# Kernel optimization log

Measured on AMD Instinct MI355X. Metric: run time of the kernel, lower is better.

## Reference

```python
import jax, jax.numpy as jnp
import numpy as np

B, S, D, H = 4, 2048, 1024, 16
DK = D // H
DFF = 4 * D
EPS = 1e-6


def setup_inputs() -> dict:
    key = jax.random.key(0)
    ks = jax.random.split(key, 16)
    s = 0.02
    return {
        "x": jax.random.normal(ks[0], (B, S, D), jnp.float32),
        "mask": jax.random.randint(ks[1], (B, 1, 1, S), 0, 2, jnp.int32),
        "wq": jax.random.normal(ks[2], (D, D), jnp.float32) * s,
        "bq": jnp.zeros((D,), jnp.float32),
        "wk": jax.random.normal(ks[3], (D, D), jnp.float32) * s,
        "bk": jnp.zeros((D,), jnp.float32),
        "wv": jax.random.normal(ks[4], (D, D), jnp.float32) * s,
        "bv": jnp.zeros((D,), jnp.float32),
        "wo": jax.random.normal(ks[5], (D, D), jnp.float32) * s,
        "bo": jnp.zeros((D,), jnp.float32),
        "w1": jax.random.normal(ks[6], (DFF, D), jnp.float32) * s,
        "b1": jnp.zeros((DFF,), jnp.float32),
        "w2": jax.random.normal(ks[7], (D, DFF), jnp.float32) * s,
        "b2": jnp.zeros((D,), jnp.float32),
        "a1": jnp.ones((1,), jnp.float32),
        "c1": jnp.zeros((1,), jnp.float32),
        "a2": jnp.ones((1,), jnp.float32),
        "c2": jnp.zeros((1,), jnp.float32),
    }


def _layernorm(x, alpha, bias):
    # source: alpha * (x - mean) / (std + eps) + bias, torch std is unbiased
    mean = jnp.mean(x, axis=-1, keepdims=True)
    std = jnp.std(x, axis=-1, keepdims=True, ddof=1)
    return alpha * (x - mean) / (std + EPS) + bias


def _mha(x, mask, wq, bq, wk, bk, wv, bv, wo, bo):
    q = (x @ wq.T + bq).reshape(B, S, H, DK).transpose(0, 2, 1, 3)  # [B,H,S,DK]
    k = (x @ wk.T + bk).reshape(B, S, H, DK).transpose(0, 2, 1, 3)
    v = (x @ wv.T + bv).reshape(B, S, H, DK).transpose(0, 2, 1, 3)
    scores = jnp.einsum("bhqd,bhkd->bhqk", q, k) / jnp.sqrt(jnp.float32(DK))
    scores = jnp.where(mask == 0, jnp.float32(-1e9), scores)
    attn = jax.nn.softmax(scores, axis=-1)
    out = jnp.einsum("bhqk,bhkd->bhqd", attn, v)  # [B,H,S,DK]
    out = out.transpose(0, 2, 1, 3).reshape(B, S, D)
    return out @ wo.T + bo


def reference(x, mask, wq, bq, wk, bk, wv, bv, wo, bo, w1, b1, w2, b2, a1, c1, a2, c2):
    # residual 1: x + MHA(LN(x))  (dropout = identity in eval)
    h = x + _mha(_layernorm(x, a1, c1), mask, wq, bq, wk, bk, wv, bv, wo, bo)
    # residual 2: h + FFN(LN(h))
    hn = _layernorm(h, a2, c2)
    ffn = jax.nn.relu(hn @ w1.T + b1) @ w2.T + b2
    return h + ffn
```

## Files before the change

### kernel.cpp

```cpp
#include <hip/hip_runtime.h>
#include <math.h>

static constexpr int B  = 4;
static constexpr int S  = 2048;
static constexpr int D  = 1024;
static constexpr int H  = 16;
static constexpr int DFF = 4096;

typedef __attribute__((ext_vector_type(8))) short short8;
typedef __attribute__((ext_vector_type(8))) unsigned short ushort8;
typedef __attribute__((ext_vector_type(4))) unsigned short ushort4v;
typedef __attribute__((ext_vector_type(4))) float f32x4;

__device__ __forceinline__ float b2f(unsigned short u) {
  unsigned int x = ((unsigned int)u) << 16;
  float f;
  __builtin_memcpy(&f, &x, 4);
  return f;
}
__device__ __forceinline__ unsigned short f2b(float f) {
  unsigned int x;
  __builtin_memcpy(&x, &f, 4);
  x += 0x7fffu + ((x >> 16) & 1u);
  return (unsigned short)(x >> 16);
}

__device__ __forceinline__ f32x4 mfma16(short8 a, short8 b, f32x4 c) {
  return __builtin_amdgcn_mfma_f32_16x16x32_bf16(a, b, c, 0, 0, 0);
}

__device__ __forceinline__ void gload_lds16(const void* gsrc, void* ldst) {
  __builtin_amdgcn_global_load_lds(
      (__attribute__((address_space(1))) void*)(uintptr_t)gsrc,
      (__attribute__((address_space(3))) void*)ldst, 16, 0, 0);
}

struct CvtArgs {
  const float* s[6];
  unsigned short* d[6];
  int n[6];
};
__global__ __launch_bounds__(256) void convert6(CvtArgs a) {
  const int seg = blockIdx.y;
  const int i = (blockIdx.x * 256 + threadIdx.x) * 4;
  if (i < a.n[seg]) {
    f32x4 v = *(const f32x4*)(a.s[seg] + i);
    ushort4v o;
#pragma unroll
    for (int j = 0; j < 4; j++) o[j] = f2b(v[j]);
    *(ushort4v*)(a.d[seg] + i) = o;
  }
}

__global__ __launch_bounds__(256) void ln_fused(const float* __restrict__ x,
                                                const float* __restrict__ ap,
                                                const float* __restrict__ cp,
                                                unsigned short* __restrict__ out) {
  const int row = blockIdx.x, tid = threadIdx.x;
  const size_t base = (size_t)row * D;
  float v[4];
  float s = 0.f, sq = 0.f;
#pragma unroll
  for (int i = 0; i < 4; i++) {
    v[i] = x[base + tid + i * 256];
    s += v[i];
    sq += v[i] * v[i];
  }
#pragma unroll
  for (int o = 32; o > 0; o >>= 1) {
    s += __shfl_xor(s, o);
    sq += __shfl_xor(sq, o);
  }
  __shared__ __align__(16) float rs[4], rq[4];
  const int wave = tid >> 6, lane = tid & 63;
  if (lane == 0) {
    rs[wave] = s;
    rq[wave] = sq;
  }
  __syncthreads();
  const float S1 = rs[0] + rs[1] + rs[2] + rs[3];
  const float S2 = rq[0] + rq[1] + rq[2] + rq[3];
  const float mean = S1 * (1.f / 1024.f);
  const float var = fmaxf(0.f, (S2 - 1024.f * mean * mean) * (1.f / 1023.f));
  const float rstd = 1.f / (sqrtf(var) + 1e-6f);
  const float alpha = ap[0], beta = cp[0];
#pragma unroll
  for (int i = 0; i < 4; i++)
    out[base + tid + i * 256] = f2b(alpha * (v[i] - mean) * rstd + beta);
}

template <int EPI>
__global__ __launch_bounds__(256) void gemm_bb(
    const unsigned short* __restrict__ A, const unsigned short* __restrict__ W,
    const float* __restrict__ bias0, const float* __restrict__ bias1,
    const float* __restrict__ bias2, const float* __restrict__ resid,
    void* __restrict__ out, unsigned short* __restrict__ outK,
    unsigned short* __restrict__ outV, int M, int N, int K, int ldw) {
  __shared__ __align__(16) unsigned short As[128 * 32];
  __shared__ __align__(16) unsigned short Bs[128 * 32];
  const int tid = threadIdx.x;
  const int lane = tid & 63, wave = tid >> 6;
  const int quad = lane >> 4, l16 = lane & 15;
  const int m0 = blockIdx.y * 128, n0 = blockIdx.x * 128;
  const int wm = (wave >> 1) * 64, wn = (wave & 1) * 64;

  f32x4 acc[4][4];
#pragma unroll
  for (int i = 0; i < 4; i++)
#pragma unroll
    for (int j = 0; j < 4; j++) acc[i][j] = {0.f, 0.f, 0.f, 0.f};

  const int rA = tid >> 2;
  const int kc = (tid & 3) * 8;

  for (int k0 = 0; k0 < K; k0 += 32) {
    __syncthreads();
#pragma unroll
    for (int i = 0; i < 2; i++) {
      const int row = i * 64 + rA;
      gload_lds16(&A[(size_t)(m0 + row) * K + k0 + kc], &As[(i * 256 + wave * 64) * 8]);
      gload_lds16(&W[(size_t)(n0 + row) * ldw + k0 + kc], &Bs[(i * 256 + wave * 64) * 8]);
    }
    __syncthreads();
    short8 af[4], bf[4];
#pragma unroll
    for (int t = 0; t < 4; t++) {
      af[t] = *(const short8*)&As[(wm + t * 16 + l16) * 32 + quad * 8];
      bf[t] = *(const short8*)&Bs[(wn + t * 16 + l16) * 32 + quad * 8];
    }
#pragma unroll
    for (int mt = 0; mt < 4; mt++)
#pragma unroll
      for (int nt = 0; nt < 4; nt++) acc[mt][nt] = mfma16(af[mt], bf[nt], acc[mt][nt]);
  }

  if (EPI == 4) {
    const int band = (n0 + wn) >> 10;
    const float* bp = band == 0 ? bias0 : (band == 1 ? bias1 : bias2);
#pragma unroll
    for (int nt = 0; nt < 4; nt++) {
      const int col = n0 + wn + nt * 16 + l16;
      const int cl = col & 1023;
      const float bv = bp[cl];
#pragma unroll
      for (int mt = 0; mt < 4; mt++) {
#pragma unroll
        for (int r = 0; r < 4; r++) {
          const int row = m0 + wm + mt * 16 + quad * 4 + r;
          const float v = acc[mt][nt][r] + bv;
          if (band == 0)
            ((unsigned short*)out)[(size_t)row * 1024 + cl] = f2b(v);
          else if (band == 1)
            outK[(size_t)row * 1024 + cl] = f2b(v);
          else
            outV[((size_t)((row >> 11) * 1024 + cl)) * 2048 + (row & 2047)] = f2b(v);
        }
      }
    }
  } else {
#pragma unroll
    for (int nt = 0; nt < 4; nt++) {
      const int col = n0 + wn + nt * 16 + l16;
      const float bv = (EPI == 3) ? 0.f : bias0[col];
#pragma unroll
      for (int mt = 0; mt < 4; mt++) {
#pragma unroll
        for (int r = 0; r < 4; r++) {
          const int row = m0 + wm + mt * 16 + quad * 4 + r;
          const size_t idx = (size_t)row * N + col;
          float v = acc[mt][nt][r] + bv;
          if (EPI == 2) {
            v = fmaxf(v, 0.f);
            ((unsigned short*)out)[idx] = f2b(v);
          } else {
            v += resid[idx];
            ((float*)out)[idx] = v;
          }
        }
      }
    }
  }
}

__global__ __launch_bounds__(256) void attn_kernel(unsigned short* __restrict__ Q,
                                                   const unsigned short* __restrict__ Kb,
                                                   const unsigned short* __restrict__ VT,
                                                   const int* __restrict__ mask) {
  constexpr int PAD = 72;
  __shared__ __align__(16) unsigned short Ks[64 * PAD];
  __shared__ __align__(16) unsigned short VTs[64 * PAD];
  __shared__ __align__(16) unsigned short Pb[4][16 * PAD];

  const int tid = threadIdx.x, lane = tid & 63, wave = tid >> 6;
  const int quad = lane >> 4, l16 = lane & 15;
  const int q0 = blockIdx.x * 64;
  const int b = blockIdx.y >> 4, h = blockIdx.y & 15;

  short8 qf0, qf1;
  {
    const int qr = q0 + wave * 16 + l16;
    const unsigned short* qp = &Q[((size_t)(b * S) + qr) * D + h * 64 + quad * 8];
    qf0 = *(const short8*)qp;
    qf1 = *(const short8*)(qp + 32);
  }

  float l_acc = 0.f;
  f32x4 o_acc[4];
#pragma unroll
  for (int t = 0; t < 4; t++) o_acc[t] = {0.f, 0.f, 0.f, 0.f};

  const int rT = tid >> 3;
  const int cT = (tid & 7) * 8;

  for (int kt = 0; kt < S / 64; kt++) {
    const int k0 = kt * 64;
    ushort8 kv[2], vv[2];
#pragma unroll
    for (int i = 0; i < 2; i++) {
      const int r = i * 32 + rT;
      kv[i] = *(const ushort8*)&Kb[((size_t)(b * S) + k0 + r) * D + h * 64 + cT];
      vv[i] = *(const ushort8*)&VT[((size_t)(blockIdx.y * 64 + r)) * S + k0 + cT];
    }
    __syncthreads();
#pragma unroll
    for (int i = 0; i < 2; i++) {
      const int r = i * 32 + rT;
      *(ushort8*)&Ks[r * PAD + cT] = kv[i];
      *(ushort8*)&VTs[r * PAD + cT] = vv[i];
    }
    __syncthreads();

    f32x4 sc[4];
#pragma unroll
    for (int nt = 0; nt < 4; nt++) sc[nt] = {0.f, 0.f, 0.f, 0.f};
#pragma unroll
    for (int nt = 0; nt < 4; nt++) {
      short8 kf0 = *(const short8*)&Ks[(nt * 16 + l16) * PAD + quad * 8];
      short8 kf1 = *(const short8*)&Ks[(nt * 16 + l16) * PAD + 32 + quad * 8];
      sc[nt] = mfma16(kf0, qf0, sc[nt]);
      sc[nt] = mfma16(kf1, qf1, sc[nt]);
    }

#pragma unroll
    for (int nt = 0; nt < 4; nt++) {
      const int4 mv = *(const int4*)&mask[b * S + k0 + nt * 16 + quad * 4];
      ushort4v pk;
      {
        const float p0 = __expf(fmaf(sc[nt][0], 0.125f, mv.x ? -12.f : -42.f));
        const float p1 = __expf(fmaf(sc[nt][1], 0.125f, mv.y ? -12.f : -42.f));
        const float p2 = __expf(fmaf(sc[nt][2], 0.125f, mv.z ? -12.f : -42.f));
        const float p3 = __expf(fmaf(sc[nt][3], 0.125f, mv.w ? -12.f : -42.f));
        l_acc += p0 + p1 + p2 + p3;
        pk[0] = f2b(p0);
        pk[1] = f2b(p1);
        pk[2] = f2b(p2);
        pk[3] = f2b(p3);
      }
      *(ushort4v*)&Pb[wave][l16 * PAD + nt * 16 + quad * 4] = pk;
    }

    short8 pf0 = *(const short8*)&Pb[wave][l16 * PAD + quad * 8];
    short8 pf1 = *(const short8*)&Pb[wave][l16 * PAD + 32 + quad * 8];
#pragma unroll
    for (int nt = 0; nt < 4; nt++) {
      short8 vf0 = *(const short8*)&VTs[(nt * 16 + l16) * PAD + quad * 8];
      short8 vf1 = *(const short8*)&VTs[(nt * 16 + l16) * PAD + 32 + quad * 8];
      o_acc[nt] = mfma16(pf0, vf0, o_acc[nt]);
      o_acc[nt] = mfma16(pf1, vf1, o_acc[nt]);
    }
  }

  l_acc += __shfl_xor(l_acc, 16);
  l_acc += __shfl_xor(l_acc, 32);

#pragma unroll
  for (int r = 0; r < 4; r++) {
    const float lr = __shfl(l_acc, quad * 4 + r);
    const float inv = 1.f / lr;
    const int q = q0 + wave * 16 + quad * 4 + r;
#pragma unroll
    for (int nt = 0; nt < 4; nt++) {
      const int dk = nt * 16 + l16;
      Q[((size_t)(b * S) + q) * D + h * 64 + dk] = f2b(o_acc[nt][r] * inv);
    }
  }
}

__global__ __launch_bounds__(256) void stats_kernel(const float* __restrict__ x,
                                                    float2* __restrict__ st) {
  const int row = blockIdx.x, tid = threadIdx.x;
  const size_t base = (size_t)row * D;
  float s = 0.f, sq = 0.f;
#pragma unroll
  for (int i = 0; i < 4; i++) {
    const float v = x[base + tid + i * 256];
    s += v;
    sq += v * v;
  }
#pragma unroll
  for (int o = 32; o > 0; o >>= 1) {
    s += __shfl_xor(s, o);
    sq += __shfl_xor(sq, o);
  }
  __shared__ __align__(16) float rs[4], rq[4];
  const int wave = tid >> 6, lane = tid & 63;
  if (lane == 0) {
    rs[wave] = s;
    rq[wave] = sq;
  }
  __syncthreads();
  if (tid == 0) {
    const float S1 = rs[0] + rs[1] + rs[2] + rs[3];
    const float S2 = rq[0] + rq[1] + rq[2] + rq[3];
    const float mean = S1 * (1.f / 1024.f);
    const float var = fmaxf(0.f, (S2 - 1024.f * mean * mean) * (1.f / 1023.f));
    const float rstd = 1.f / (sqrtf(var) + 1e-6f);
    st[row] = make_float2(mean, rstd);
  }
}

template <int EPI, int NORM, int AF32, int OUTF32>
__global__ __launch_bounds__(256) void gemm_bt(
    const void* __restrict__ Ap, const float* __restrict__ W,
    const float* __restrict__ bias, const float* __restrict__ resid,
    void* __restrict__ outp, const float2* __restrict__ stats,
    const float* __restrict__ alpha_p, const float* __restrict__ beta_p,
    int M, int N, int K, int ldw) {
  __shared__ __align__(16) unsigned short As[128 * 32];
  __shared__ __align__(16) unsigned short Bs[128 * 32];
  const int tid = threadIdx.x;
  const int lane = tid & 63, wave = tid >> 6;
  const int quad = lane >> 4, l16 = lane & 15;
  const int m0 = blockIdx.y * 128, n0 = blockIdx.x * 128;
  const int wm = (wave >> 1) * 64, wn = (wave & 1) * 64;

  float alpha = 0.f, beta = 0.f;
  if (NORM) {
    alpha = alpha_p[0];
    beta = beta_p[0];
  }

  f32x4 acc[4][4];
#pragma unroll
  for (int i = 0; i < 4; i++)
#pragma unroll
    for (int j = 0; j < 4; j++) acc[i][j] = {0.f, 0.f, 0.f, 0.f};

  const int rA = tid >> 2;
  const int kc = (tid & 3) * 8;

  for (int k0 = 0; k0 < K; k0 += 32) {
    ushort8 av[2], bv8[2];
#pragma unroll
    for (int i = 0; i < 2; i++) {
      const int row = i * 64 + rA;
      if (AF32) {
        const float* ap = (const float*)Ap + (size_t)(m0 + row) * K + k0 + kc;
        f32x4 a0 = *(const f32x4*)ap;
        f32x4 a1 = *(const f32x4*)(ap + 4);
        if (NORM) {
          const float2 st = stats[m0 + row];
#pragma unroll
          for (int j = 0; j < 4; j++) {
            a0[j] = alpha * (a0[j] - st.x) * st.y + beta;
            a1[j] = alpha * (a1[j] - st.x) * st.y + beta;
          }
        }
#pragma unroll
        for (int j = 0; j < 4; j++) {
          av[i][j] = f2b(a0[j]);
          av[i][j + 4] = f2b(a1[j]);
        }
      } else {
        av[i] = *(const ushort8*)((const unsigned short*)Ap +
                                  (size_t)(m0 + row) * K + k0 + kc);
      }
      const float* wp = W + (size_t)(n0 + row) * ldw + k0 + kc;
      f32x4 w0 = *(const f32x4*)wp;
      f32x4 w1 = *(const f32x4*)(wp + 4);
#pragma unroll
      for (int j = 0; j < 4; j++) {
        bv8[i][j] = f2b(w0[j]);
        bv8[i][j + 4] = f2b(w1[j]);
      }
    }
    __syncthreads();
#pragma unroll
    for (int i = 0; i < 2; i++) {
      const int row = i * 64 + rA;
      *(ushort8*)&As[row * 32 + kc] = av[i];
      *(ushort8*)&Bs[row * 32 + kc] = bv8[i];
    }
    __syncthreads();
    short8 af[4], bf[4];
#pragma unroll
    for (int t = 0; t < 4; t++) {
      af[t] = *(const short8*)&As[(wm + t * 16 + l16) * 32 + quad * 8];
      bf[t] = *(const short8*)&Bs[(wn + t * 16 + l16) * 32 + quad * 8];
    }
#pragma unroll
    for (int mt = 0; mt < 4; mt++)
#pragma unroll
      for (int nt = 0; nt < 4; nt++) acc[mt][nt] = mfma16(af[mt], bf[nt], acc[mt][nt]);
  }

#pragma unroll
  for (int nt = 0; nt < 4; nt++) {
    const int col = n0 + wn + nt * 16 + l16;
    const float bv = (EPI == 3) ? 0.f : bias[col];
#pragma unroll
    for (int mt = 0; mt < 4; mt++) {
#pragma unroll
      for (int r = 0; r < 4; r++) {
        const int row = m0 + wm + mt * 16 + quad * 4 + r;
        float v = acc[mt][nt][r] + bv;
        if (EPI == 2) v = fmaxf(v, 0.f);
        if (EPI == 4) {
          const size_t vtidx =
              ((size_t)((row >> 11) * 1024 + col)) * 2048 + (row & 2047);
          ((unsigned short*)outp)[vtidx] = f2b(v);
        } else {
          const size_t idx = (size_t)row * N + col;
          if (EPI == 1 || EPI == 3) v += resid[idx];
          if (OUTF32)
            ((float*)outp)[idx] = v;
          else
            ((unsigned short*)outp)[idx] = f2b(v);
        }
      }
    }
  }
}

extern "C" void kernel_launch(void* const* d_in, const int* in_sizes, int n_in,
                              void* d_out, int out_size, void* d_ws, size_t ws_size,
                              hipStream_t stream) {
  (void)in_sizes; (void)n_in; (void)out_size;
  const float* x  = (const float*)d_in[0];
  const int* mask = (const int*)d_in[1];
  const float* wq = (const float*)d_in[2];
  const float* bq = (const float*)d_in[3];
  const float* wk = (const float*)d_in[4];
  const float* bk = (const float*)d_in[5];
  const float* wv = (const float*)d_in[6];
  const float* bv = (const float*)d_in[7];
  const float* wo = (const float*)d_in[8];
  const float* bo = (const float*)d_in[9];
  const float* w1 = (const float*)d_in[10];
  const float* b1 = (const float*)d_in[11];
  const float* w2 = (const float*)d_in[12];
  const float* b2 = (const float*)d_in[13];
  const float* a1 = (const float*)d_in[14];
  const float* c1 = (const float*)d_in[15];
  const float* a2 = (const float*)d_in[16];
  const float* c2 = (const float*)d_in[17];

  char* ws = (char*)d_ws;
  const size_t MB = 1 << 20;
  const int M = B * S;
  dim3 blk(256);
  dim3 gAttn(S / 64, B * H);

  if (ws_size >= 89 * MB) {
    const int tier3 = (ws_size >= 152 * MB);
    const int tier2 = (ws_size >= 121 * MB);
    unsigned short* wqkv_b = (unsigned short*)(ws + 0);
    unsigned short* wo_b   = (unsigned short*)(ws + 6 * MB);
    unsigned short* w1_b   = (unsigned short*)(ws + 8 * MB);
    unsigned short* w2_b   = (unsigned short*)(ws + 16 * MB);
    unsigned short* ln1x   = (unsigned short*)(ws + 25 * MB);
    unsigned short* q      = (unsigned short*)(ws + 41 * MB);
    unsigned short* kk     = (unsigned short*)(ws + 57 * MB);
    unsigned short* vt     = (unsigned short*)(ws + 73 * MB);
    float*          hbuf   = (float*)(ws + 57 * MB);
    unsigned short* ln2x   = (unsigned short*)(ws + 25 * MB);
    unsigned short* ffn1q  = (unsigned short*)(ws + 41 * MB);
    unsigned short* ffn1h  = (unsigned short*)(ws + 89 * MB);
    unsigned short* ffn1f  = (unsigned short*)(ws + 89 * MB);
    float* outb = (float*)d_out;

    CvtArgs ca;
    ca.s[0] = wq; ca.d[0] = wqkv_b;            ca.n[0] = 1048576;
    ca.s[1] = wk; ca.d[1] = wqkv_b + 1048576;  ca.n[1] = 1048576;
    ca.s[2] = wv; ca.d[2] = wqkv_b + 2097152;  ca.n[2] = 1048576;
    ca.s[3] = wo; ca.d[3] = wo_b;              ca.n[3] = 1048576;
    ca.s[4] = w1; ca.d[4] = w1_b;              ca.n[4] = 4194304;
    ca.s[5] = w2; ca.d[5] = w2_b;              ca.n[5] = 4194304;
    convert6<<<dim3(4096, 6), blk, 0, stream>>>(ca);

    ln_fused<<<M, blk, 0, stream>>>(x, a1, c1, ln1x);
    gemm_bb<4><<<dim3(24, 64), blk, 0, stream>>>(ln1x, wqkv_b, bq, bk, bv, nullptr,
                                                 q, kk, vt, M, 3072, D, D);
    attn_kernel<<<gAttn, blk, 0, stream>>>(q, kk, vt, mask);
    gemm_bb<1><<<dim3(8, 64), blk, 0, stream>>>(q, wo_b, bo, nullptr, nullptr, x,
                                                hbuf, nullptr, nullptr, M, D, D, D);
    ln_fused<<<M, blk, 0, stream>>>(hbuf, a2, c2, ln2x);

    if (tier3) {
      gemm_bb<2><<<dim3(32, 64), blk, 0, stream>>>(ln2x, w1_b, b1, nullptr, nullptr,
                                                   nullptr, ffn1f, nullptr, nullptr,
                                                   M, DFF, D, D);
      gemm_bb<1><<<dim3(8, 64), blk, 0, stream>>>(ffn1f, w2_b, b2, nullptr, nullptr,
                                                  hbuf, outb, nullptr, nullptr,
                                                  M, D, DFF, DFF);
    } else if (tier2) {
      gemm_bb<2><<<dim3(16, 64), blk, 0, stream>>>(ln2x, w1_b, b1, nullptr, nullptr,
                                                   nullptr, ffn1h, nullptr, nullptr,
                                                   M, 2048, D, D);
      gemm_bb<1><<<dim3(8, 64), blk, 0, stream>>>(ffn1h, w2_b, b2, nullptr, nullptr,
                                                  hbuf, outb, nullptr, nullptr,
                                                  M, D, 2048, DFF);
      gemm_bb<2><<<dim3(16, 64), blk, 0, stream>>>(ln2x, w1_b + (size_t)2048 * D,
                                                   b1 + 2048, nullptr, nullptr, nullptr,
                                                   ffn1h, nullptr, nullptr, M, 2048, D, D);
      gemm_bb<3><<<dim3(8, 64), blk, 0, stream>>>(ffn1h, w2_b + 2048, nullptr, nullptr,
                                                  nullptr, outb, outb, nullptr, nullptr,
                                                  M, D, 2048, DFF);
    } else {
      for (int i = 0; i < 4; i++) {
        gemm_bb<2><<<dim3(8, 64), blk, 0, stream>>>(ln2x, w1_b + (size_t)i * 1024 * D,
                                                    b1 + i * 1024, nullptr, nullptr,
                                                    nullptr, ffn1q, nullptr, nullptr,
                                                    M, 1024, D, D);
        if (i == 0)
          gemm_bb<1><<<dim3(8, 64), blk, 0, stream>>>(ffn1q, w2_b + i * 1024, b2, nullptr,
                                                      nullptr, hbuf, outb, nullptr, nullptr,
                                                      M, D, 1024, DFF);
        else
          gemm_bb<3><<<dim3(8, 64), blk, 0, stream>>>(ffn1q, w2_b + i * 1024, nullptr,
                                                      nullptr, nullptr, outb, outb, nullptr,
                                                      nullptr, M, D, 1024, DFF);
      }
    }
  } else {
    float2* stats1 = (float2*)(ws + 0);
    float2* stats2 = (float2*)(ws + 128 * 1024);
    unsigned short* q    = (unsigned short*)(ws + 1 * MB);
    unsigned short* kk   = (unsigned short*)(ws + 17 * MB);
    unsigned short* vt   = (unsigned short*)(ws + 33 * MB);
    float*          hbuf = (float*)(ws + 17 * MB);
    unsigned short* ffn1 = (unsigned short*)(ws + 1 * MB);
    float* outb = (float*)d_out;
    dim3 gD(D / 128, M / 128);

    stats_kernel<<<M, blk, 0, stream>>>(x, stats1);
    gemm_bt<0, 1, 1, 0><<<gD, blk, 0, stream>>>(x, wq, bq, nullptr, q, stats1, a1, c1, M, D, D, D);
    gemm_bt<0, 1, 1, 0><<<gD, blk, 0, stream>>>(x, wk, bk, nullptr, kk, stats1, a1, c1, M, D, D, D);
    gemm_bt<4, 1, 1, 0><<<gD, blk, 0, stream>>>(x, wv, bv, nullptr, vt, stats1, a1, c1, M, D, D, D);
    attn_kernel<<<gAttn, blk, 0, stream>>>(q, kk, vt, mask);
    gemm_bt<1, 0, 0, 1><<<gD, blk, 0, stream>>>(q, wo, bo, x, hbuf, nullptr, nullptr, nullptr, M, D, D, D);
    stats_kernel<<<M, blk, 0, stream>>>(hbuf, stats2);
    for (int i = 0; i < 4; i++) {
      gemm_bt<2, 1, 1, 0><<<gD, blk, 0, stream>>>(hbuf, w1 + (size_t)i * 1024 * D,
                                                  b1 + i * 1024, nullptr, ffn1, stats2,
                                                  a2, c2, M, 1024, D, D);
      if (i == 0)
        gemm_bt<1, 0, 0, 1><<<gD, blk, 0, stream>>>(ffn1, w2 + i * 1024, b2, hbuf, outb,
                                                    nullptr, nullptr, nullptr, M, D, 1024, DFF);
      else
        gemm_bt<3, 0, 0, 1><<<gD, blk, 0, stream>>>(ffn1, w2 + i * 1024, nullptr, outb, outb,
                                                    nullptr, nullptr, nullptr, M, D, 1024, DFF);
    }
  }
}
```

Before: 630.8 us.

## Add 256x256 double-buffered ping-pong GEMM for QKV and FFN1 projections

Adds a new 512-thread GEMM kernel with 256x256 output tiles, 64-wide K steps, double-buffered LDS filled by direct global-to-LDS loads, XOR swizzled layout, an XCD-aware workgroup remap, and barrier-interleaved MFMA phases with s_setprio. It replaces the 128x128 GEMM for the QKV projection and the first FFN GEMM (tier3 path), aiming at more data reuse per tile and better overlap of loads with matrix math. It also raises wave priority around the MFMA sections in the attention kernel. The larger tiles produce fewer workgroups, which may leave some compute units underused, and the hand-placed waitcnts make correctness depend on the exact ordering of the loads.

```diff
diff --git a/kernel.cpp b/kernel.cpp
--- a/kernel.cpp
+++ b/kernel.cpp
@@ -34,6 +34,14 @@
       (__attribute__((address_space(1))) void*)(uintptr_t)gsrc,
       (__attribute__((address_space(3))) void*)ldst, 16, 0, 0);
 }
+
+#define LGK0 asm volatile("s_waitcnt lgkmcnt(0)" ::: "memory")
+#define VMC8 asm volatile("s_waitcnt vmcnt(8)" ::: "memory")
+#define VMC0 asm volatile("s_waitcnt vmcnt(0)" ::: "memory")
+#define SB0  __builtin_amdgcn_sched_barrier(0)
+#define BAR  __builtin_amdgcn_s_barrier()
+#define PRIO1 __builtin_amdgcn_s_setprio(1)
+#define PRIO0 __builtin_amdgcn_s_setprio(0)
 
 struct CvtArgs {
   const float* s[6];
@@ -87,6 +95,179 @@
 #pragma unroll
   for (int i = 0; i < 4; i++)
     out[base + tid + i * 256] = f2b(alpha * (v[i] - mean) * rstd + beta);
+}
+
+__device__ __forceinline__ void stage_tile(const unsigned short* pA0,
+                                           const unsigned short* pB0,
+                                           unsigned short* ldsbuf, int wave,
+                                           size_t K64, int koff) {
+#pragma unroll
+  for (int j = 0; j < 4; j++)
+    gload_lds16(pA0 + j * K64 + koff, ldsbuf + j * 4096 + wave * 512);
+#pragma unroll
+  for (int j = 0; j < 4; j++)
+    gload_lds16(pB0 + j * K64 + koff, ldsbuf + 16384 + j * 4096 + wave * 512);
+}
+
+template <int EPI>
+__global__ __launch_bounds__(512, 2) void gemm256(
+    const unsigned short* __restrict__ A, const unsigned short* __restrict__ W,
+    const float* __restrict__ bias0, const float* __restrict__ bias1,
+    const float* __restrict__ bias2, void* __restrict__ out,
+    unsigned short* __restrict__ outK, unsigned short* __restrict__ outV,
+    int M, int N, int K) {
+  __shared__ __align__(16) unsigned short lds[2 * 32768];
+  const int tid = threadIdx.x;
+  const int lane = tid & 63, wave = tid >> 6;
+  const int quad = lane >> 4, l16 = lane & 15;
+
+  const int nbx = gridDim.x;
+  const int nwg = nbx * gridDim.y;
+  int wg = blockIdx.y * nbx + blockIdx.x;
+  if (!(nwg & 7)) wg = (wg & 7) * (nwg >> 3) + (wg >> 3);
+  const int bx = wg % nbx, by = wg / nbx;
+  const int m0 = by * 256, n0 = bx * 256;
+  const int wm = wave >> 2, wn = wave & 3;
+
+  const int srow = wave * 8 + (lane >> 3);
+  const int scol = ((lane & 7) ^ (lane >> 3)) * 8;
+  const size_t K64 = (size_t)K * 64;
+  const unsigned short* pA0 = A + (size_t)(m0 + srow) * K + scol;
+  const unsigned short* pB0 = W + (size_t)(n0 + srow) * K + scol;
+
+  const int xr = l16 & 7;
+  const int aoff0 = ((0 + quad) ^ xr) * 8;
+  const int aoff1 = ((4 + quad) ^ xr) * 8;
+  const int arow = wm * 128 + l16;
+  const int brow = wn * 64 + l16;
+
+  f32x4 acc[8][4];
+#pragma unroll
+  for (int i = 0; i < 8; i++)
+#pragma unroll
+    for (int j = 0; j < 4; j++) acc[i][j] = {0.f, 0.f, 0.f, 0.f};
+
+  const int nkt = K >> 6;
+  stage_tile(pA0, pB0, &lds[0], wave, K64, 0);
+  stage_tile(pA0, pB0, &lds[32768], wave, K64, 64);
+  VMC8;
+  SB0;
+  BAR;
+
+  short8 af[4][2], bf[4][2];
+  for (int t = 0; t < nkt; ++t) {
+    const int p = t & 1;
+    const unsigned short* Ab = &lds[p * 32768];
+    const unsigned short* Bb = Ab + 16384;
+
+#pragma unroll
+    for (int nt = 0; nt < 4; nt++) {
+      bf[nt][0] = *(const short8*)&Bb[(brow + nt * 16) * 64 + aoff0];
+      bf[nt][1] = *(const short8*)&Bb[(brow + nt * 16) * 64 + aoff1];
+    }
+#pragma unroll
+    for (int mt = 0; mt < 4; mt++) {
+      af[mt][0] = *(const short8*)&Ab[(arow + mt * 16) * 64 + aoff0];
+      af[mt][1] = *(const short8*)&Ab[(arow + mt * 16) * 64 + aoff1];
+    }
+    BAR;
+    LGK0;
+    SB0;
+    PRIO1;
+#pragma unroll
+    for (int mt = 0; mt < 4; mt++)
+#pragma unroll
+      for (int nt = 0; nt < 2; nt++) {
+        acc[mt][nt] = mfma16(af[mt][0], bf[nt][0], acc[mt][nt]);
+        acc[mt][nt] = mfma16(af[mt][1], bf[nt][1], acc[mt][nt]);
+      }
+    PRIO0;
+    BAR;
+    PRIO1;
+#pragma unroll
+    for (int mt = 0; mt < 4; mt++)
+#pragma unroll
+      for (int nt = 2; nt < 4; nt++) {
+        acc[mt][nt] = mfma16(af[mt][0], bf[nt][0], acc[mt][nt]);
+        acc[mt][nt] = mfma16(af[mt][1], bf[nt][1], acc[mt][nt]);
+      }
+    PRIO0;
+    BAR;
+#pragma unroll
+    for (int i = 0; i < 4; i++) {
+      af[i][0] = *(const short8*)&Ab[(arow + 64 + i * 16) * 64 + aoff0];
+      af[i][1] = *(const short8*)&Ab[(arow + 64 + i * 16) * 64 + aoff1];
+    }
+    LGK0;
+    SB0;
+    BAR;
+    if (t + 2 < nkt) stage_tile(pA0, pB0, &lds[p * 32768], wave, K64, (t + 2) * 64);
+    PRIO1;
+#pragma unroll
+    for (int i = 0; i < 4; i++)
+#pragma unroll
+      for (int nt = 0; nt < 2; nt++) {
+        acc[4 + i][nt] = mfma16(af[i][0], bf[nt][0], acc[4 + i][nt]);
+        acc[4 + i][nt] = mfma16(af[i][1], bf[nt][1], acc[4 + i][nt]);
+      }
+    PRIO0;
+    BAR;
+    PRIO1;
+#pragma unroll
+    for (int i = 0; i < 4; i++)
+#pragma unroll
+      for (int nt = 2; nt < 4; nt++) {
+        acc[4 + i][nt] = mfma16(af[i][0], bf[nt][0], acc[4 + i][nt]);
+        acc[4 + i][nt] = mfma16(af[i][1], bf[nt][1], acc[4 + i][nt]);
+      }
+    PRIO0;
+    if (t + 2 < nkt) {
+      VMC8;
+    } else if (t + 1 < nkt) {
+      VMC0;
+    }
+    SB0;
+    BAR;
+  }
+
+  if (EPI == 4) {
+    const int band = (n0 + wn * 64) >> 10;
+    const float* bp = band == 0 ? bias0 : (band == 1 ? bias1 : bias2);
+#pragma unroll
+    for (int nt = 0; nt < 4; nt++) {
+      const int col = n0 + wn * 64 + nt * 16 + l16;
+      const int cl = col & 1023;
+      const float bv = bp[cl];
+#pragma unroll
+      for (int mt = 0; mt < 8; mt++) {
+#pragma unroll
+        for (int r = 0; r < 4; r++) {
+          const int row = m0 + wm * 128 + mt * 16 + quad * 4 + r;
+          const float v = acc[mt][nt][r] + bv;
+          if (band == 0)
+            ((unsigned short*)out)[(size_t)row * 1024 + cl] = f2b(v);
+          else if (band == 1)
+            outK[(size_t)row * 1024 + cl] = f2b(v);
+          else
+            outV[((size_t)((row >> 11) * 1024 + cl)) * 2048 + (row & 2047)] = f2b(v);
+        }
+      }
+    }
+  } else {
+#pragma unroll
+    for (int nt = 0; nt < 4; nt++) {
+      const int col = n0 + wn * 64 + nt * 16 + l16;
+      const float bv = bias0[col];
+#pragma unroll
+      for (int mt = 0; mt < 8; mt++)
+#pragma unroll
+        for (int r = 0; r < 4; r++) {
+          const int row = m0 + wm * 128 + mt * 16 + quad * 4 + r;
+          ((unsigned short*)out)[(size_t)row * (size_t)N + col] =
+              f2b(fmaxf(acc[mt][nt][r] + bv, 0.f));
+        }
+    }
+  }
 }
 
 template <int EPI>
@@ -233,6 +414,7 @@
     f32x4 sc[4];
 #pragma unroll
     for (int nt = 0; nt < 4; nt++) sc[nt] = {0.f, 0.f, 0.f, 0.f};
+    PRIO1;
 #pragma unroll
     for (int nt = 0; nt < 4; nt++) {
       short8 kf0 = *(const short8*)&Ks[(nt * 16 + l16) * PAD + quad * 8];
@@ -240,6 +422,7 @@
       sc[nt] = mfma16(kf0, qf0, sc[nt]);
       sc[nt] = mfma16(kf1, qf1, sc[nt]);
     }
+    PRIO0;
 
 #pragma unroll
     for (int nt = 0; nt < 4; nt++) {
@@ -261,6 +444,7 @@
 
     short8 pf0 = *(const short8*)&Pb[wave][l16 * PAD + quad * 8];
     short8 pf1 = *(const short8*)&Pb[wave][l16 * PAD + 32 + quad * 8];
+    PRIO1;
 #pragma unroll
     for (int nt = 0; nt < 4; nt++) {
       short8 vf0 = *(const short8*)&VTs[(nt * 16 + l16) * PAD + quad * 8];
@@ -268,6 +452,7 @@
       o_acc[nt] = mfma16(pf0, vf0, o_acc[nt]);
       o_acc[nt] = mfma16(pf1, vf1, o_acc[nt]);
     }
+    PRIO0;
   }
 
   l_acc += __shfl_xor(l_acc, 16);
@@ -459,6 +644,7 @@
   const size_t MB = 1 << 20;
   const int M = B * S;
   dim3 blk(256);
+  dim3 blk512(512);
   dim3 gAttn(S / 64, B * H);
 
   if (ws_size >= 89 * MB) {
@@ -489,17 +675,17 @@
     convert6<<<dim3(4096, 6), blk, 0, stream>>>(ca);
 
     ln_fused<<<M, blk, 0, stream>>>(x, a1, c1, ln1x);
-    gemm_bb<4><<<dim3(24, 64), blk, 0, stream>>>(ln1x, wqkv_b, bq, bk, bv, nullptr,
-                                                 q, kk, vt, M, 3072, D, D);
+    gemm256<4><<<dim3(12, 32), blk512, 0, stream>>>(ln1x, wqkv_b, bq, bk, bv,
+                                                    q, kk, vt, M, 3072, D);
     attn_kernel<<<gAttn, blk, 0, stream>>>(q, kk, vt, mask);
     gemm_bb<1><<<dim3(8, 64), blk, 0, stream>>>(q, wo_b, bo, nullptr, nullptr, x,
                                                 hbuf, nullptr, nullptr, M, D, D, D);
     ln_fused<<<M, blk, 0, stream>>>(hbuf, a2, c2, ln2x);
 
     if (tier3) {
-      gemm_bb<2><<<dim3(32, 64), blk, 0, stream>>>(ln2x, w1_b, b1, nullptr, nullptr,
-                                                   nullptr, ffn1f, nullptr, nullptr,
-                                                   M, DFF, D, D);
+      gemm256<2><<<dim3(16, 32), blk512, 0, stream>>>(ln2x, w1_b, b1, nullptr,
+                                                      nullptr, ffn1f, nullptr,
+                                                      nullptr, M, DFF, D);
       gemm_bb<1><<<dim3(8, 64), blk, 0, stream>>>(ffn1f, w2_b, b2, nullptr, nullptr,
                                                   hbuf, outb, nullptr, nullptr,
                                                   M, D, DFF, DFF);
```

Result: no change. 628.2 us (-0.4%).

## Load attention K/V tiles directly to LDS with XOR swizzle

Applied to the files above, without the earlier changes.

The attention kernel now stages each K and V^T tile with global_load_lds straight into unpadded, XOR-swizzled shared memory. This replaces the register round trip and padded layout, and uses raw barriers plus an explicit vmcnt wait. It also adds s_setprio around the MFMA sections and packs the probability conversion to bf16 with v_cvt_pk_bf16_f32. The goal is to cut register pressure, LDS store instructions and bank conflicts in the inner loop. The load is still not double-buffered, so each iteration waits for its global loads before computing.

```diff
diff --git a/kernel.cpp b/kernel.cpp
--- a/kernel.cpp
+++ b/kernel.cpp
@@ -25,6 +25,12 @@
   return (unsigned short)(x >> 16);
 }
 
+__device__ __forceinline__ unsigned int cvtpk_bf16(float lo, float hi) {
+  unsigned int r;
+  asm("v_cvt_pk_bf16_f32 %0, %1, %2" : "=v"(r) : "v"(lo), "v"(hi));
+  return r;
+}
+
 __device__ __forceinline__ f32x4 mfma16(short8 a, short8 b, f32x4 c) {
   return __builtin_amdgcn_mfma_f32_16x16x32_bf16(a, b, c, 0, 0, 0);
 }
@@ -34,6 +40,12 @@
       (__attribute__((address_space(1))) void*)(uintptr_t)gsrc,
       (__attribute__((address_space(3))) void*)ldst, 16, 0, 0);
 }
+
+#define VMC0 asm volatile("s_waitcnt vmcnt(0)" ::: "memory")
+#define SB0  __builtin_amdgcn_sched_barrier(0)
+#define BAR  __builtin_amdgcn_s_barrier()
+#define PRIO1 __builtin_amdgcn_s_setprio(1)
+#define PRIO0 __builtin_amdgcn_s_setprio(0)
 
 struct CvtArgs {
   const float* s[6];
@@ -182,19 +194,36 @@
   }
 }
 
+__device__ __forceinline__ void attn_stage(const unsigned short* Kg,
+                                           const unsigned short* Vg,
+                                           unsigned short* Kd, unsigned short* Vd,
+                                           int kt) {
+  gload_lds16(Kg + (size_t)kt * 64 * D, Kd);
+  gload_lds16(Kg + (size_t)kt * 64 * D + 8 * (size_t)D, Kd + 8 * 64);
+  gload_lds16(Vg + (size_t)kt * 64, Vd);
+  gload_lds16(Vg + (size_t)kt * 64 + 8 * (size_t)S, Vd + 8 * 64);
+}
+
 __global__ __launch_bounds__(256) void attn_kernel(unsigned short* __restrict__ Q,
                                                    const unsigned short* __restrict__ Kb,
                                                    const unsigned short* __restrict__ VT,
                                                    const int* __restrict__ mask) {
-  constexpr int PAD = 72;
-  __shared__ __align__(16) unsigned short Ks[64 * PAD];
-  __shared__ __align__(16) unsigned short VTs[64 * PAD];
-  __shared__ __align__(16) unsigned short Pb[4][16 * PAD];
+  __shared__ __align__(16) unsigned short Ks[64 * 64];
+  __shared__ __align__(16) unsigned short Vs[64 * 64];
+  constexpr int PPAD = 72;
+  __shared__ __align__(16) unsigned short Pb[4][16 * PPAD];
 
   const int tid = threadIdx.x, lane = tid & 63, wave = tid >> 6;
   const int quad = lane >> 4, l16 = lane & 15;
   const int q0 = blockIdx.x * 64;
   const int b = blockIdx.y >> 4, h = blockIdx.y & 15;
+
+  const int sr = lane >> 3;
+  const int sc8 = ((lane & 7) ^ sr) * 8;
+  const unsigned short* Kg = Kb + ((size_t)b * S + wave * 16 + sr) * D + h * 64 + sc8;
+  const unsigned short* Vg = VT + ((size_t)blockIdx.y * 64 + wave * 16 + sr) * S + sc8;
+  unsigned short* Kd = &Ks[(wave * 16) * 64];
+  unsigned short* Vd = &Vs[(wave * 16) * 64];
 
   short8 qf0, qf1;
   {
@@ -209,65 +238,56 @@
 #pragma unroll
   for (int t = 0; t < 4; t++) o_acc[t] = {0.f, 0.f, 0.f, 0.f};
 
-  const int rT = tid >> 3;
-  const int cT = (tid & 7) * 8;
+  const int xr = l16 & 7;
+  const int c0 = (quad ^ xr) * 8;
+  const int c1 = ((quad + 4) ^ xr) * 8;
 
   for (int kt = 0; kt < S / 64; kt++) {
     const int k0 = kt * 64;
-    ushort8 kv[2], vv[2];
-#pragma unroll
-    for (int i = 0; i < 2; i++) {
-      const int r = i * 32 + rT;
-      kv[i] = *(const ushort8*)&Kb[((size_t)(b * S) + k0 + r) * D + h * 64 + cT];
-      vv[i] = *(const ushort8*)&VT[((size_t)(blockIdx.y * 64 + r)) * S + k0 + cT];
-    }
-    __syncthreads();
-#pragma unroll
-    for (int i = 0; i < 2; i++) {
-      const int r = i * 32 + rT;
-      *(ushort8*)&Ks[r * PAD + cT] = kv[i];
-      *(ushort8*)&VTs[r * PAD + cT] = vv[i];
-    }
-    __syncthreads();
-
-    f32x4 sc[4];
-#pragma unroll
-    for (int nt = 0; nt < 4; nt++) sc[nt] = {0.f, 0.f, 0.f, 0.f};
+    BAR;
+    attn_stage(Kg, Vg, Kd, Vd, kt);
+    VMC0;
+    SB0;
+    BAR;
+
+    f32x4 sc4[4];
+#pragma unroll
+    for (int nt = 0; nt < 4; nt++) sc4[nt] = {0.f, 0.f, 0.f, 0.f};
+    PRIO1;
 #pragma unroll
     for (int nt = 0; nt < 4; nt++) {
-      short8 kf0 = *(const short8*)&Ks[(nt * 16 + l16) * PAD + quad * 8];
-      short8 kf1 = *(const short8*)&Ks[(nt * 16 + l16) * PAD + 32 + quad * 8];
-      sc[nt] = mfma16(kf0, qf0, sc[nt]);
-      sc[nt] = mfma16(kf1, qf1, sc[nt]);
-    }
+      short8 kf0 = *(const short8*)&Ks[(nt * 16 + l16) * 64 + c0];
+      short8 kf1 = *(const short8*)&Ks[(nt * 16 + l16) * 64 + c1];
+      sc4[nt] = mfma16(kf0, qf0, sc4[nt]);
+      sc4[nt] = mfma16(kf1, qf1, sc4[nt]);
+    }
+    PRIO0;
 
 #pragma unroll
     for (int nt = 0; nt < 4; nt++) {
       const int4 mv = *(const int4*)&mask[b * S + k0 + nt * 16 + quad * 4];
-      ushort4v pk;
-      {
-        const float p0 = __expf(fmaf(sc[nt][0], 0.125f, mv.x ? -12.f : -42.f));
-        const float p1 = __expf(fmaf(sc[nt][1], 0.125f, mv.y ? -12.f : -42.f));
-        const float p2 = __expf(fmaf(sc[nt][2], 0.125f, mv.z ? -12.f : -42.f));
-        const float p3 = __expf(fmaf(sc[nt][3], 0.125f, mv.w ? -12.f : -42.f));
-        l_acc += p0 + p1 + p2 + p3;
-        pk[0] = f2b(p0);
-        pk[1] = f2b(p1);
-        pk[2] = f2b(p2);
-        pk[3] = f2b(p3);
-      }
-      *(ushort4v*)&Pb[wave][l16 * PAD + nt * 16 + quad * 4] = pk;
-    }
-
-    short8 pf0 = *(const short8*)&Pb[wave][l16 * PAD + quad * 8];
-    short8 pf1 = *(const short8*)&Pb[wave][l16 * PAD + 32 + quad * 8];
+      const float p0 = __expf(fmaf(sc4[nt][0], 0.125f, mv.x ? -12.f : -42.f));
+      const float p1 = __expf(fmaf(sc4[nt][1], 0.125f, mv.y ? -12.f : -42.f));
+      const float p2 = __expf(fmaf(sc4[nt][2], 0.125f, mv.z ? -12.f : -42.f));
+      const float p3 = __expf(fmaf(sc4[nt][3], 0.125f, mv.w ? -12.f : -42.f));
+      l_acc += (p0 + p1) + (p2 + p3);
+      uint2 pw;
+      pw.x = cvtpk_bf16(p0, p1);
+      pw.y = cvtpk_bf16(p2, p3);
+      *(uint2*)&Pb[wave][l16 * PPAD + nt * 16 + quad * 4] = pw;
+    }
+
+    short8 pf0 = *(const short8*)&Pb[wave][l16 * PPAD + quad * 8];
+    short8 pf1 = *(const short8*)&Pb[wave][l16 * PPAD + 32 + quad * 8];
+    PRIO1;
 #pragma unroll
     for (int nt = 0; nt < 4; nt++) {
-      short8 vf0 = *(const short8*)&VTs[(nt * 16 + l16) * PAD + quad * 8];
-      short8 vf1 = *(const short8*)&VTs[(nt * 16 + l16) * PAD + 32 + quad * 8];
+      short8 vf0 = *(const short8*)&Vs[(nt * 16 + l16) * 64 + c0];
+      short8 vf1 = *(const short8*)&Vs[(nt * 16 + l16) * 64 + c1];
       o_acc[nt] = mfma16(pf0, vf0, o_acc[nt]);
       o_acc[nt] = mfma16(pf1, vf1, o_acc[nt]);
     }
+    PRIO0;
   }
 
   l_acc += __shfl_xor(l_acc, 16);
```

Result: faster. 605.9 us (-4.0%).
